# Kernel optimization log

Hardware: AMD Instinct MI355X
Metric: run time of the kernel (lower is better)

The kernel has to match this reference:

```python
import jax, jax.numpy as jnp
import numpy as np
from functools import partial

L, H, D, HD, V, S_MAX = 12, 12, 768, 64, 50257, 1024
EPS = 1e-5


def _layernorm(x, g, b):
    m = jnp.mean(x, axis=-1, keepdims=True)
    v = jnp.mean(jnp.square(x - m), axis=-1, keepdims=True)
    return (x - m) * jax.lax.rsqrt(v + EPS) * g + b


def setup_inputs() -> dict:
    key = jax.random.key(0)
    ks = jax.random.split(key, 8)
    s = 0.02
    return {
        "input_ids": jax.random.randint(ks[0], (2, 1024), 0, V),
        "wte": jax.random.normal(ks[1], (V, D), jnp.float32) * s,
        "wpe": jax.random.normal(ks[2], (S_MAX, D), jnp.float32) * s,
        "ln1_g": jnp.ones((L, D), jnp.float32),
        "ln1_b": jnp.zeros((L, D), jnp.float32),
        "Wqkv": jax.random.normal(ks[3], (L, D, 3 * D), jnp.float32) * s,
        "bqkv": jnp.zeros((L, 3 * D), jnp.float32),
        "Wo": jax.random.normal(ks[4], (L, D, D), jnp.float32) * s,
        "bo": jnp.zeros((L, D), jnp.float32),
        "ln2_g": jnp.ones((L, D), jnp.float32),
        "ln2_b": jnp.zeros((L, D), jnp.float32),
        "Wfc": jax.random.normal(ks[5], (L, D, 4 * D), jnp.float32) * s,
        "bfc": jnp.zeros((L, 4 * D), jnp.float32),
        "Wp": jax.random.normal(ks[6], (L, 4 * D, D), jnp.float32) * s,
        "bp": jnp.zeros((L, D), jnp.float32),
        "lnf_g": jnp.ones((D,), jnp.float32),
        "lnf_b": jnp.zeros((D,), jnp.float32),
    }


def reference(input_ids, wte, wpe, ln1_g, ln1_b, Wqkv, bqkv, Wo, bo,
              ln2_g, ln2_b, Wfc, bfc, Wp, bp, lnf_g, lnf_b):
    B, S = input_ids.shape
    x = wte[input_ids] + wpe[:S][None]  # [B,S,D] (embd dropout = identity in eval)
    causal = jnp.tril(jnp.ones((S, S), bool))  # [S,S]
    scale = 1.0 / jnp.sqrt(jnp.asarray(HD, x.dtype))

    def block(x, p):
        l1g, l1b, wqkv, bq, wo, bo_, l2g, l2b, wfc, bfc_, wp, bp_ = p
        h = _layernorm(x, l1g, l1b)
        qkv = h @ wqkv + bq  # [B,S,3D]
        q, k, v = jnp.split(qkv, 3, axis=-1)
        q = q.reshape(B, S, H, HD).transpose(0, 2, 1, 3)  # [B,H,S,HD]
        k = k.reshape(B, S, H, HD).transpose(0, 2, 1, 3)
        v = v.reshape(B, S, H, HD).transpose(0, 2, 1, 3)
        scores = jnp.einsum('bhqd,bhkd->bhqk', q, k) * scale  # [B,H,S,S]
        scores = jnp.where(causal, scores, -jnp.inf)
        attn = jax.nn.softmax(scores, axis=-1)  # attn dropout = identity in eval
        o = jnp.einsum('bhqk,bhkd->bhqd', attn, v)
        o = o.transpose(0, 2, 1, 3).reshape(B, S, D)
        x = x + (o @ wo + bo_)
        h2 = _layernorm(x, l2g, l2b)
        m = jax.nn.gelu(h2 @ wfc + bfc_, approximate=False)  # exact erf GELU
        x = x + (m @ wp + bp_)
        return x, None

    params = (ln1_g, ln1_b, Wqkv, bqkv, Wo, bo, ln2_g, ln2_b, Wfc, bfc, Wp, bp)
    x, _ = jax.lax.scan(block, x, params)
    x = _layernorm(x, lnf_g, lnf_b)
    logits = jnp.einsum('bsd,vd->bsv', x, wte)  # tied lm_head, no bias
    return logits
```

## Files before the change

kernel.cpp:

```cpp
#include <hip/hip_runtime.h>
#include <hip/hip_bf16.h>
#include <hip/hip_fp16.h>


typedef __attribute__((ext_vector_type(8))) short short8;
typedef __attribute__((ext_vector_type(4))) float f32x4;

#define S_LEN  1024
#define NTOK   2048
#define DMODEL 768
#define NHEAD  12
#define HEADD  64
#define NLAYER 12
#define VOCAB  50257
#define DQKV   2304
#define DFF    3072

__device__ __forceinline__ unsigned short f2bf(float f) {
  unsigned u = __float_as_uint(f);
  u += 0x7fffu + ((u >> 16) & 1u);
  return (unsigned short)(u >> 16);
}
__device__ __forceinline__ unsigned short f2h(float f) {
  __half h = __float2half(f);
  return *reinterpret_cast<unsigned short*>(&h);
}

__device__ __forceinline__ f32x4 mfma_bf16(short8 a, short8 b, f32x4 c) {
  asm("v_mfma_f32_16x16x32_bf16 %0, %1, %2, %0" : "+v"(c) : "v"(a), "v"(b));
  return c;
}
__device__ __forceinline__ f32x4 mfma_f16(short8 a, short8 b, f32x4 c) {
  asm("v_mfma_f32_16x16x32_f16 %0, %1, %2, %0" : "+v"(c) : "v"(a), "v"(b));
  return c;
}

__device__ __forceinline__ void gll16(const void* g, void* l) {
  __builtin_amdgcn_global_load_lds(
      (const __attribute__((address_space(1))) void*)g,
      (__attribute__((address_space(3))) void*)l, 16, 0, 0);
}

__global__ __launch_bounds__(256) void embed_kernel(
    const int* __restrict__ ids, const float* __restrict__ wte,
    const float* __restrict__ wpe, float* __restrict__ x) {
  int i = blockIdx.x * 256 + threadIdx.x;
  int n = i / DMODEL, d = i - n * DMODEL;
  int s = n & (S_LEN - 1);
  x[i] = wte[(long)ids[n] * DMODEL + d] + wpe[(long)s * DMODEL + d];
}

__global__ __launch_bounds__(256) void convert_kernel(
    const float* __restrict__ in, unsigned short* __restrict__ out, long n4) {
  long i = (long)blockIdx.x * 256 + threadIdx.x;
  if (i >= n4) return;
  float4 v = ((const float4*)in)[i];
  ushort4 r;
  r.x = f2bf(v.x); r.y = f2bf(v.y); r.z = f2bf(v.z); r.w = f2bf(v.w);
  ((ushort4*)out)[i] = r;
}

__global__ __launch_bounds__(256) void transpose_kernel(
    const float* __restrict__ in, unsigned short* __restrict__ out, int R, int C,
    long ldin, long ldout) {
  in  += (long)blockIdx.z * ldin;
  out += (long)blockIdx.z * ldout;
  __shared__ float tile[32][33];
  int tx = threadIdx.x & 31, ty = threadIdx.x >> 5;
  int c0 = blockIdx.x * 32, r0 = blockIdx.y * 32;
#pragma unroll
  for (int i = 0; i < 4; ++i) {
    int r = r0 + ty + i * 8;
    tile[ty + i * 8][tx] = in[(long)r * C + c0 + tx];
  }
  __syncthreads();
#pragma unroll
  for (int i = 0; i < 4; ++i) {
    int orow = c0 + ty + i * 8;
    out[(long)orow * R + r0 + tx] = f2bf(tile[tx][ty + i * 8]);
  }
}

__global__ __launch_bounds__(256) void ln_kernel(
    const float* __restrict__ x, const float* __restrict__ g,
    const float* __restrict__ b, unsigned short* __restrict__ out) {
  __shared__ float sb[4];
  int n = blockIdx.x, t = threadIdx.x;
  const float* xr = x + (long)n * DMODEL;
  float v0 = xr[t], v1 = xr[t + 256], v2 = xr[t + 512];
  float sum = v0 + v1 + v2;
#pragma unroll
  for (int o = 32; o; o >>= 1) sum += __shfl_xor(sum, o);
  if ((t & 63) == 0) sb[t >> 6] = sum;
  __syncthreads();
  sum = sb[0] + sb[1] + sb[2] + sb[3];
  float mean = sum * (1.f / 768.f);
  float d0 = v0 - mean, d1 = v1 - mean, d2 = v2 - mean;
  float vs = d0 * d0 + d1 * d1 + d2 * d2;
#pragma unroll
  for (int o = 32; o; o >>= 1) vs += __shfl_xor(vs, o);
  __syncthreads();
  if ((t & 63) == 0) sb[t >> 6] = vs;
  __syncthreads();
  vs = sb[0] + sb[1] + sb[2] + sb[3];
  float rs = rsqrtf(vs * (1.f / 768.f) + 1e-5f);
  out[(long)n * DMODEL + t]       = f2bf(d0 * rs * g[t] + b[t]);
  out[(long)n * DMODEL + t + 256] = f2bf(d1 * rs * g[t + 256] + b[t + 256]);
  out[(long)n * DMODEL + t + 512] = f2bf(d2 * rs * g[t + 512] + b[t + 512]);
}

__global__ __launch_bounds__(256) void attn_kernel(
    const unsigned short* __restrict__ qkv, unsigned short* __restrict__ o_out) {
  __shared__ __align__(16) unsigned short Ks[64 * 64];
  __shared__ __align__(16) unsigned short Vt[64 * 64];
  __shared__ __align__(16) unsigned short Ps[4][16 * 72];
  int t = threadIdx.x, w = t >> 6, l = t & 63;
  int qtile = gridDim.x - 1 - blockIdx.x;
  int bh = blockIdx.y;
  int b = bh / NHEAD, h = bh - b * NHEAD;
  long nb = (long)b * S_LEN;
  int g = l >> 4, lr = l & 15;

  int q0 = qtile * 64 + w * 16;
  const unsigned short* qrow = qkv + (nb + q0 + lr) * (long)DQKV + h * HEADD;
  short8 qf0 = *(const short8*)(qrow + g * 8);
  short8 qf1 = *(const short8*)(qrow + 32 + g * 8);

  f32x4 O[4];
  f32x4 zero = {0.f, 0.f, 0.f, 0.f};
#pragma unroll
  for (int jt = 0; jt < 4; ++jt) O[jt] = zero;
  float m[4] = {-INFINITY, -INFINITY, -INFINITY, -INFINITY};
  float ls[4] = {0.f, 0.f, 0.f, 0.f};

  int skey = t >> 2;
  int sd0 = (t & 3) * 16;
  int nt = qtile + 1;
  for (int c = 0; c < nt; ++c) {
    int k0 = c * 64;
    __syncthreads();
    {
      int c0 = t, row = c0 >> 3, j = c0 & 7;
      long goff = (nb + k0 + row) * (long)DQKV + DMODEL + h * HEADD + ((j ^ (row & 7)) * 8);
      gll16(qkv + goff, (char*)Ks + c0 * 16);
      int c1 = t + 256; row = c1 >> 3; j = c1 & 7;
      goff = (nb + k0 + row) * (long)DQKV + DMODEL + h * HEADD + ((j ^ (row & 7)) * 8);
      gll16(qkv + goff, (char*)Ks + c1 * 16);
    }
    {
      const unsigned short* vr =
          qkv + (nb + k0 + skey) * (long)DQKV + 2 * DMODEL + h * HEADD + sd0;
      short8 v0 = *(const short8*)vr;
      short8 v1 = *(const short8*)(vr + 8);
#pragma unroll
      for (int j = 0; j < 8; ++j) {
        int dv = sd0 + j;
        *(unsigned short*)((char*)Vt + dv * 128 + ((skey * 2) ^ ((dv & 7) << 4))) =
            (unsigned short)v0[j];
        dv = sd0 + 8 + j;
        *(unsigned short*)((char*)Vt + dv * 128 + ((skey * 2) ^ ((dv & 7) << 4))) =
            (unsigned short)v1[j];
      }
    }
    __syncthreads();

    f32x4 S[4];
    __builtin_amdgcn_s_setprio(1);
#pragma unroll
    for (int kt = 0; kt < 4; ++kt) {
      int krow = kt * 16 + lr;
      int o0 = (g * 16) ^ ((krow & 7) << 4);
      int o1 = (64 + g * 16) ^ ((krow & 7) << 4);
      short8 kf0 = *(const short8*)((char*)Ks + krow * 128 + o0);
      short8 kf1 = *(const short8*)((char*)Ks + krow * 128 + o1);
      S[kt] = mfma_f16(qf0, kf0, zero);
      S[kt] = mfma_f16(qf1, kf1, S[kt]);
    }
    __builtin_amdgcn_s_setprio(0);

    bool diag = (c == qtile);
    float sv[4][4];
#pragma unroll
    for (int kt = 0; kt < 4; ++kt)
#pragma unroll
      for (int r = 0; r < 4; ++r) {
        float xv = S[kt][r] * 0.125f;
        if (diag) {
          int key = kt * 16 + lr;
          int qq = w * 16 + g * 4 + r;
          if (key > qq) xv = -INFINITY;
        }
        sv[kt][r] = xv;
      }
    float nm[4], al[4];
#pragma unroll
    for (int r = 0; r < 4; ++r) {
      float mx = fmaxf(fmaxf(sv[0][r], sv[1][r]), fmaxf(sv[2][r], sv[3][r]));
#pragma unroll
      for (int o = 8; o; o >>= 1) mx = fmaxf(mx, __shfl_xor(mx, o));
      nm[r] = fmaxf(m[r], mx);
      al[r] = __expf(m[r] - nm[r]);
      m[r] = nm[r];
    }
    float rs[4] = {0.f, 0.f, 0.f, 0.f};
#pragma unroll
    for (int kt = 0; kt < 4; ++kt)
#pragma unroll
      for (int r = 0; r < 4; ++r) {
        float p = __expf(sv[kt][r] - nm[r]);
        rs[r] += p;
        Ps[w][(g * 4 + r) * 72 + kt * 16 + lr] = f2h(p);
      }
#pragma unroll
    for (int r = 0; r < 4; ++r) {
#pragma unroll
      for (int o = 8; o; o >>= 1) rs[r] += __shfl_xor(rs[r], o);
      ls[r] = ls[r] * al[r] + rs[r];
    }
#pragma unroll
    for (int jt = 0; jt < 4; ++jt) {
      f32x4 ov = O[jt];
#pragma unroll
      for (int r = 0; r < 4; ++r) ov[r] *= al[r];
      O[jt] = ov;
    }
    __builtin_amdgcn_s_setprio(1);
#pragma unroll
    for (int kk = 0; kk < 2; ++kk) {
      short8 pf = *(const short8*)(&Ps[w][lr * 72 + kk * 32 + g * 8]);
#pragma unroll
      for (int jt = 0; jt < 4; ++jt) {
        int dv = jt * 16 + lr;
        short8 vf = *(const short8*)((char*)Vt + dv * 128 +
                                     (((kk * 64 + g * 16)) ^ ((dv & 7) << 4)));
        O[jt] = mfma_f16(pf, vf, O[jt]);
      }
    }
    __builtin_amdgcn_s_setprio(0);
  }

  __syncthreads();
#pragma unroll
  for (int jt = 0; jt < 4; ++jt)
#pragma unroll
    for (int r = 0; r < 4; ++r) {
      int qq = w * 16 + g * 4 + r;
      int dv = jt * 16 + lr;
      *(unsigned short*)((char*)Ks + qq * 128 + ((dv * 2) ^ ((qq & 7) << 4))) =
          f2bf(O[jt][r] / ls[r]);
    }
  __syncthreads();
  {
    int qq = t >> 2, d0 = (t & 3) * 16;
    short8 o0 = *(const short8*)((char*)Ks + qq * 128 + ((d0 * 2) ^ ((qq & 7) << 4)));
    short8 o1 = *(const short8*)((char*)Ks + qq * 128 + (((d0 + 8) * 2) ^ ((qq & 7) << 4)));
    unsigned short* orow = o_out + (nb + qtile * 64 + qq) * (long)DMODEL + h * HEADD + d0;
    *(short8*)orow = o0;
    *(short8*)(orow + 8) = o1;
  }
}

template <int TM, int TN, int HAS_BIAS, int ACT_GELU, int RESID, int OUT_BF16,
          int OUT_F16, int COLG, int GRIDSWAP, int XCDSWZ>
__global__ __launch_bounds__(TM == 128 ? 256 : 128) void gemm_bt_kernel(
    const short* __restrict__ A, const short* __restrict__ Bt,
    const float* __restrict__ bias, float* __restrict__ Cf,
    unsigned short* __restrict__ Cb, int K, int Nv) {
  __shared__ __align__(16) short As[2][TM * 32];
  __shared__ __align__(16) short Bs[2][TN * 32];
  constexpr int NJ = (TN == 64) ? 2 : 4;
  constexpr int WN = (TN == 64) ? 32 : 64;
  int t = threadIdx.x;
  int lane = t & 63, wave = t >> 6;
  int wm = (TM == 128) ? (wave >> 1) : 0;
  int wn = (TM == 128) ? (wave & 1) : wave;

  int bx = blockIdx.x, by = blockIdx.y;
  if (XCDSWZ) {
    int gx = gridDim.x;
    int nwg = gx * gridDim.y;
    int wg = by * gx + bx;
    int q8 = nwg >> 3, r8 = nwg & 7;
    int xcd = wg & 7, idx = wg >> 3;
    int nid = (xcd < r8 ? xcd * (q8 + 1) : r8 * (q8 + 1) + (xcd - r8) * q8) + idx;
    bx = nid % gx;
    by = nid / gx;
  }
  int row0 = (GRIDSWAP ? bx : by) * TM;
  int col0 = (GRIDSWAP ? by : bx) * TN;
  int lr = lane & 15, lk = (lane >> 4) * 8;

  f32x4 acc[4][NJ];
  f32x4 zero = {0.f, 0.f, 0.f, 0.f};
#pragma unroll
  for (int i = 0; i < 4; ++i)
#pragma unroll
    for (int j = 0; j < NJ; ++j) acc[i][j] = zero;

  int rr = t >> 2, k8 = (t & 3) * 8;

  if (TM == 128) {
    int ar0 = row0 + rr, ar1 = ar0 + 64;
    int br0 = col0 + rr, br1 = br0 + 64;
    if (COLG) { br0 = min(br0, Nv - 1); br1 = min(br1, Nv - 1); }
    const short* Ap0 = A + (long)ar0 * K + k8;
    const short* Ap1 = A + (long)ar1 * K + k8;
    const short* Bp0 = Bt + (long)br0 * K + k8;
    const short* Bp1 = Bt + (long)br1 * K + k8;
    for (int kt = 0; kt < K; kt += 64) {
      __syncthreads();
#pragma unroll
      for (int s = 0; s < 2; ++s) {
        int ko = kt + s * 32;
        gll16(Ap0 + ko, (char*)As[s] + t * 16);
        gll16(Ap1 + ko, (char*)As[s] + 4096 + t * 16);
        gll16(Bp0 + ko, (char*)Bs[s] + t * 16);
        gll16(Bp1 + ko, (char*)Bs[s] + 4096 + t * 16);
      }
      __syncthreads();
#pragma unroll
      for (int s = 0; s < 2; ++s) {
        short8 af[4], bfr[4];
#pragma unroll
        for (int i = 0; i < 4; ++i) {
          af[i]  = *(const short8*)(As[s] + (wm * 64 + i * 16 + lr) * 32 + lk);
          bfr[i] = *(const short8*)(Bs[s] + (wn * 64 + i * 16 + lr) * 32 + lk);
        }
#pragma unroll
        for (int i = 0; i < 4; ++i)
#pragma unroll
          for (int j = 0; j < 4; ++j)
            acc[i][j] = mfma_bf16(af[i], bfr[j], acc[i][j]);
      }
    }
  } else if (TN == 128) {
    const short* Ap = A + (long)(row0 + rr) * K + k8;
    const short* Bp = Bt + (long)(col0 + rr) * K + k8;
    for (int kt = 0; kt < K; kt += 64) {
      __syncthreads();
#pragma unroll
      for (int s = 0; s < 2; ++s) {
        int ko = kt + s * 32;
        gll16(Ap + ko, (char*)As[s] + t * 16);
        gll16(Ap + (long)32 * K + ko, (char*)As[s] + 2048 + t * 16);
        gll16(Bp + ko, (char*)Bs[s] + t * 16);
        gll16(Bp + (long)32 * K + ko, (char*)Bs[s] + 2048 + t * 16);
        gll16(Bp + (long)64 * K + ko, (char*)Bs[s] + 4096 + t * 16);
        gll16(Bp + (long)96 * K + ko, (char*)Bs[s] + 6144 + t * 16);
      }
      __syncthreads();
#pragma unroll
      for (int s = 0; s < 2; ++s) {
        short8 af[4], bfr[4];
#pragma unroll
        for (int i = 0; i < 4; ++i) {
          af[i]  = *(const short8*)(As[s] + (i * 16 + lr) * 32 + lk);
          bfr[i] = *(const short8*)(Bs[s] + (wn * 64 + i * 16 + lr) * 32 + lk);
        }
#pragma unroll
        for (int i = 0; i < 4; ++i)
#pragma unroll
          for (int j = 0; j < 4; ++j)
            acc[i][j] = mfma_bf16(af[i], bfr[j], acc[i][j]);
      }
    }
  } else {
    const short* Ap = A + (long)(row0 + rr) * K + k8;
    const short* Bp = Bt + (long)(col0 + rr) * K + k8;
    for (int kt = 0; kt < K; kt += 64) {
      __syncthreads();
#pragma unroll
      for (int s = 0; s < 2; ++s) {
        int ko = kt + s * 32;
        gll16(Ap + ko, (char*)As[s] + t * 16);
        gll16(Ap + (long)32 * K + ko, (char*)As[s] + 2048 + t * 16);
        gll16(Bp + ko, (char*)Bs[s] + t * 16);
        gll16(Bp + (long)32 * K + ko, (char*)Bs[s] + 2048 + t * 16);
      }
      __syncthreads();
#pragma unroll
      for (int s = 0; s < 2; ++s) {
        short8 af[4], bfr[2];
#pragma unroll
        for (int i = 0; i < 4; ++i)
          af[i] = *(const short8*)(As[s] + (i * 16 + lr) * 32 + lk);
#pragma unroll
        for (int j = 0; j < 2; ++j)
          bfr[j] = *(const short8*)(Bs[s] + (wn * 32 + j * 16 + lr) * 32 + lk);
#pragma unroll
        for (int i = 0; i < 4; ++i)
#pragma unroll
          for (int j = 0; j < 2; ++j)
            acc[i][j] = mfma_bf16(af[i], bfr[j], acc[i][j]);
      }
    }
  }

  int orow = row0 + wm * 64 + (lane >> 4) * 4;
  int ocol = col0 + wn * WN + lr;
#pragma unroll
  for (int i = 0; i < 4; ++i) {
#pragma unroll
    for (int j = 0; j < NJ; ++j) {
      int col = ocol + j * 16;
      if (COLG && col >= Nv) continue;
      float bv = 0.f;
      if (HAS_BIAS) bv = bias[col];
#pragma unroll
      for (int r = 0; r < 4; ++r) {
        float xv = acc[i][j][r] + bv;
        if (ACT_GELU) xv = 0.5f * xv * (1.f + erff(xv * 0.70710678118654752f));
        long idx = (long)(orow + i * 16 + r) * Nv + col;
        if (RESID) {
          Cf[idx] += xv;
        } else if (OUT_F16) {
          Cb[idx] = f2h(xv);
        } else if (OUT_BF16) {
          Cb[idx] = f2bf(xv);
        } else {
          Cf[idx] = xv;
        }
      }
    }
  }
}

extern "C" void kernel_launch(void* const* d_in, const int* in_sizes, int n_in,
                              void* d_out, int out_size, void* d_ws, size_t ws_size,
                              hipStream_t stream) {
  const int*   ids  = (const int*)d_in[0];
  const float* wte  = (const float*)d_in[1];
  const float* wpe  = (const float*)d_in[2];
  const float* ln1g = (const float*)d_in[3];
  const float* ln1b = (const float*)d_in[4];
  const float* Wqkv = (const float*)d_in[5];
  const float* bqkv = (const float*)d_in[6];
  const float* Wo   = (const float*)d_in[7];
  const float* bo   = (const float*)d_in[8];
  const float* ln2g = (const float*)d_in[9];
  const float* ln2b = (const float*)d_in[10];
  const float* Wfc  = (const float*)d_in[11];
  const float* bfc  = (const float*)d_in[12];
  const float* Wp   = (const float*)d_in[13];
  const float* bp   = (const float*)d_in[14];
  const float* lnfg = (const float*)d_in[15];
  const float* lnfb = (const float*)d_in[16];
  float* out = (float*)d_out;

  size_t off = 0;
  auto carve = [&](size_t bytes) {
    void* p = (char*)d_ws + off;
    off += (bytes + 255) & ~(size_t)255;
    return p;
  };
  float* x = (float*)carve((size_t)NTOK * DMODEL * 4);
  unsigned short* qkvb = (unsigned short*)carve((size_t)NTOK * DQKV * 2);
  unsigned short* h    = (unsigned short*)carve((size_t)NTOK * DMODEL * 2);
  unsigned short* ob   = (unsigned short*)carve((size_t)NTOK * DMODEL * 2);
  unsigned short* mb   = (unsigned short*)carve((size_t)NTOK * DFF * 2);
  unsigned short* wteb = (unsigned short*)carve((size_t)VOCAB * DMODEL * 2);

  const size_t szQ = (size_t)DMODEL * DQKV * 2, szO = (size_t)DMODEL * DMODEL * 2;
  const size_t szF = (size_t)DMODEL * DFF * 2,  szP = (size_t)DFF * DMODEL * 2;
  size_t fixed_end = off;
  size_t full_need = fixed_end + NLAYER * (szQ + szO + szF + szP) + 4 * 256;
  bool full = ws_size >= full_need;

  unsigned short *tQ, *tO, *tF, *tP;
  if (full) {
    tQ = (unsigned short*)carve(NLAYER * szQ);
    tO = (unsigned short*)carve(NLAYER * szO);
    tF = (unsigned short*)carve(NLAYER * szF);
    tP = (unsigned short*)carve(NLAYER * szP);
  } else {
    tQ = (unsigned short*)carve(szQ);
    tO = (unsigned short*)carve(szO);
    tF = (unsigned short*)carve(szF);
    tP = (unsigned short*)carve(szP);
  }
  if (off > ws_size) return;

  dim3 blk(256), blk128(128);
  long n4 = (long)VOCAB * DMODEL / 4;
  convert_kernel<<<dim3((unsigned)((n4 + 255) / 256)), blk, 0, stream>>>(wte, wteb, n4);
  embed_kernel<<<dim3(NTOK * DMODEL / 256), blk, 0, stream>>>(ids, wte, wpe, x);

  if (full) {
    transpose_kernel<<<dim3(DQKV / 32, DMODEL / 32, NLAYER), blk, 0, stream>>>(
        Wqkv, tQ, DMODEL, DQKV, (long)DMODEL * DQKV, (long)DMODEL * DQKV);
    transpose_kernel<<<dim3(DMODEL / 32, DMODEL / 32, NLAYER), blk, 0, stream>>>(
        Wo, tO, DMODEL, DMODEL, (long)DMODEL * DMODEL, (long)DMODEL * DMODEL);
    transpose_kernel<<<dim3(DFF / 32, DMODEL / 32, NLAYER), blk, 0, stream>>>(
        Wfc, tF, DMODEL, DFF, (long)DMODEL * DFF, (long)DMODEL * DFF);
    transpose_kernel<<<dim3(DMODEL / 32, DFF / 32, NLAYER), blk, 0, stream>>>(
        Wp, tP, DFF, DMODEL, (long)DFF * DMODEL, (long)DFF * DMODEL);
  }

  for (int l = 0; l < NLAYER; ++l) {
    const unsigned short* tQl = tQ + (full ? (size_t)l * DMODEL * DQKV : 0);
    const unsigned short* tOl = tO + (full ? (size_t)l * DMODEL * DMODEL : 0);
    const unsigned short* tFl = tF + (full ? (size_t)l * DMODEL * DFF : 0);
    const unsigned short* tPl = tP + (full ? (size_t)l * DFF * DMODEL : 0);
    if (!full) {
      transpose_kernel<<<dim3(DQKV / 32, DMODEL / 32), blk, 0, stream>>>(
          Wqkv + (long)l * DMODEL * DQKV, tQ, DMODEL, DQKV, 0, 0);
      transpose_kernel<<<dim3(DMODEL / 32, DMODEL / 32), blk, 0, stream>>>(
          Wo + (long)l * DMODEL * DMODEL, tO, DMODEL, DMODEL, 0, 0);
      transpose_kernel<<<dim3(DFF / 32, DMODEL / 32), blk, 0, stream>>>(
          Wfc + (long)l * DMODEL * DFF, tF, DMODEL, DFF, 0, 0);
      transpose_kernel<<<dim3(DMODEL / 32, DFF / 32), blk, 0, stream>>>(
          Wp + (long)l * DFF * DMODEL, tP, DFF, DMODEL, 0, 0);
    }

    ln_kernel<<<dim3(NTOK), blk, 0, stream>>>(x, ln1g + l * DMODEL, ln1b + l * DMODEL, h);
    gemm_bt_kernel<64, 64, 1, 0, 0, 0, 1, 0, 0, 0>
        <<<dim3(DQKV / 64, NTOK / 64), blk128, 0, stream>>>(
        (const short*)h, (const short*)tQl, bqkv + (long)l * DQKV,
        nullptr, qkvb, DMODEL, DQKV);

    attn_kernel<<<dim3(S_LEN / 64, 2 * NHEAD), blk, 0, stream>>>(qkvb, ob);

    gemm_bt_kernel<64, 64, 1, 0, 1, 0, 0, 0, 0, 0>
        <<<dim3(DMODEL / 64, NTOK / 64), blk128, 0, stream>>>(
        (const short*)ob, (const short*)tOl, bo + (long)l * DMODEL,
        x, nullptr, DMODEL, DMODEL);

    ln_kernel<<<dim3(NTOK), blk, 0, stream>>>(x, ln2g + l * DMODEL, ln2b + l * DMODEL, h);
    gemm_bt_kernel<64, 64, 1, 1, 0, 1, 0, 0, 0, 0>
        <<<dim3(DFF / 64, NTOK / 64), blk128, 0, stream>>>(
        (const short*)h, (const short*)tFl, bfc + (long)l * DFF,
        nullptr, mb, DMODEL, DFF);

    gemm_bt_kernel<64, 64, 1, 0, 1, 0, 0, 0, 0, 0>
        <<<dim3(DMODEL / 64, NTOK / 64), blk128, 0, stream>>>(
        (const short*)mb, (const short*)tPl, bp + (long)l * DMODEL,
        x, nullptr, DFF, DMODEL);
  }

  ln_kernel<<<dim3(NTOK), blk, 0, stream>>>(x, lnfg, lnfb, h);
  gemm_bt_kernel<128, 128, 0, 0, 0, 0, 0, 1, 1, 1>
      <<<dim3(NTOK / 128, (VOCAB + 127) / 128), blk, 0, stream>>>(
      (const short*)h, (const short*)wteb, nullptr, out, nullptr, DMODEL, VOCAB);
}
```

Baseline: 2.227 ms.

## Double-buffer LDS tiles in 64x64 GEMM path to overlap loads with MFMA

The 64x64 tile GEMM path gets a second pair of LDS buffers. The next K-slice is issued with global-to-LDS loads before the current slice is computed, using partial vmcnt waits and raw s_barriers in place of two __syncthreads per iteration. The aim is to hide global memory latency behind the MFMA work. In exchange the kernel uses twice the LDS, which may lower occupancy, and it depends on hand-written waitcnt counts being correct.

```diff
diff --git a/kernel.cpp b/kernel.cpp
--- a/kernel.cpp
+++ b/kernel.cpp
@@ -266,8 +266,9 @@
     const short* __restrict__ A, const short* __restrict__ Bt,
     const float* __restrict__ bias, float* __restrict__ Cf,
     unsigned short* __restrict__ Cb, int K, int Nv) {
-  __shared__ __align__(16) short As[2][TM * 32];
-  __shared__ __align__(16) short Bs[2][TN * 32];
+  constexpr int NB = (TM == 64 && TN == 64) ? 2 : 1;
+  __shared__ __align__(16) short As[NB * 2][TM * 32];
+  __shared__ __align__(16) short Bs[NB * 2][TN * 32];
   constexpr int NJ = (TN == 64) ? 2 : 4;
   constexpr int WN = (TN == 64) ? 32 : 64;
   int t = threadIdx.x;
@@ -367,32 +368,44 @@
   } else {
     const short* Ap = A + (long)(row0 + rr) * K + k8;
     const short* Bp = Bt + (long)(col0 + rr) * K + k8;
+    auto issue8 = [&](int bsel, int kb) {
+#pragma unroll
+      for (int s = 0; s < 2; ++s) {
+        int ko = kb + s * 32;
+        gll16(Ap + ko, (char*)As[bsel * 2 + s] + t * 16);
+        gll16(Ap + (long)32 * K + ko, (char*)As[bsel * 2 + s] + 2048 + t * 16);
+        gll16(Bp + ko, (char*)Bs[bsel * 2 + s] + t * 16);
+        gll16(Bp + (long)32 * K + ko, (char*)Bs[bsel * 2 + s] + 2048 + t * 16);
+      }
+    };
+    issue8(0, 0);
+    int cur = 0;
     for (int kt = 0; kt < K; kt += 64) {
-      __syncthreads();
-#pragma unroll
-      for (int s = 0; s < 2; ++s) {
-        int ko = kt + s * 32;
-        gll16(Ap + ko, (char*)As[s] + t * 16);
-        gll16(Ap + (long)32 * K + ko, (char*)As[s] + 2048 + t * 16);
-        gll16(Bp + ko, (char*)Bs[s] + t * 16);
-        gll16(Bp + (long)32 * K + ko, (char*)Bs[s] + 2048 + t * 16);
-      }
-      __syncthreads();
+      if (kt + 64 < K) {
+        issue8(cur ^ 1, kt + 64);
+        asm volatile("s_waitcnt vmcnt(8)" ::: "memory");
+      } else {
+        asm volatile("s_waitcnt vmcnt(0)" ::: "memory");
+      }
+      __builtin_amdgcn_sched_barrier(0);
+      __builtin_amdgcn_s_barrier();
 #pragma unroll
       for (int s = 0; s < 2; ++s) {
         short8 af[4], bfr[2];
 #pragma unroll
         for (int i = 0; i < 4; ++i)
-          af[i] = *(const short8*)(As[s] + (i * 16 + lr) * 32 + lk);
+          af[i] = *(const short8*)(As[cur * 2 + s] + (i * 16 + lr) * 32 + lk);
 #pragma unroll
         for (int j = 0; j < 2; ++j)
-          bfr[j] = *(const short8*)(Bs[s] + (wn * 32 + j * 16 + lr) * 32 + lk);
+          bfr[j] = *(const short8*)(Bs[cur * 2 + s] + (wn * 32 + j * 16 + lr) * 32 + lk);
 #pragma unroll
         for (int i = 0; i < 4; ++i)
 #pragma unroll
           for (int j = 0; j < 2; ++j)
             acc[i][j] = mfma_bf16(af[i], bfr[j], acc[i][j]);
       }
+      __builtin_amdgcn_s_barrier();
+      cur ^= 1;
     }
   }
 
```

Measured after the change: 2.395 ms. 7.6% more time.
